# Kernel optimization log

Hardware: AMD Instinct MI355X
Metric: run time of the kernel (lower is better)

The kernel has to match this reference:

```python
import jax, jax.numpy as jnp
import numpy as np

WINDOW = 4
EPS = 1e-5


def setup_inputs() -> dict:
    key = jax.random.key(0)
    ks = jax.random.split(key, 12)
    B, T, D = 2, 4096, 1024
    H = D // 2
    s = 0.02
    return {
        "x": jax.random.normal(ks[0], (B, T, D), dtype=jnp.float32),
        # tension_net: Linear(2D -> D/2), SiLU, Linear(D/2 -> 1). Weights stored [in, out].
        "w1": jax.random.normal(ks[1], (2 * D, H), dtype=jnp.float32) * s,
        "b1": jnp.zeros((H,), dtype=jnp.float32),
        "w2": jax.random.normal(ks[2], (H, 1), dtype=jnp.float32) * s,
        "b2": jnp.zeros((1,), dtype=jnp.float32),
        # wv: Linear(D -> D)
        "wv_w": jax.random.normal(ks[3], (D, D), dtype=jnp.float32) * s,
        "wv_b": jnp.zeros((D,), dtype=jnp.float32),
        # merge: Linear(2D -> D)
        "merge_w": jax.random.normal(ks[4], (2 * D, D), dtype=jnp.float32) * s,
        "merge_b": jnp.zeros((D,), dtype=jnp.float32),
        # LayerNorm(D)
        "gamma": jnp.ones((D,), dtype=jnp.float32),
        "beta": jnp.zeros((D,), dtype=jnp.float32),
    }


def reference(x, w1, b1, w2, b2, wv_w, wv_b, merge_w, merge_b, gamma, beta):
    B, T, D = x.shape
    W = WINDOW
    # Causal sliding-window neighbor gather: nb[:, t, w] = x[:, t-w-1] if t-w-1 >= 0 else 0.
    idx = jnp.arange(T)[:, None] - jnp.arange(W)[None, :] - 1          # [T, W]
    valid = (idx >= 0)                                                  # [T, W]
    nb = jnp.take(x, jnp.clip(idx, 0, None), axis=1)                   # [B, T, W, D]
    nb = jnp.where(valid[None, :, :, None], nb, jnp.zeros((), x.dtype))
    # Pairwise tension gate: tiny MLP on [h_t, nb].
    h_t = jnp.broadcast_to(x[:, :, None, :], (B, T, W, D))
    pair = jnp.concatenate([h_t, nb], axis=-1)                          # [B, T, W, 2D]
    hid = jax.nn.silu(jnp.einsum('btwe,eh->btwh', pair, w1) + b1)       # [B, T, W, D/2]
    tau = jax.nn.sigmoid((jnp.einsum('btwh,ho->btwo', hid, w2) + b2)[..., 0])  # [B, T, W]
    # Value projection of neighbors (note: zero-padded neighbors still get wv bias, matching torch).
    v = jnp.einsum('btwd,de->btwe', nb, wv_w) + wv_b                    # [B, T, W, D]
    msg = jnp.einsum('btw,btwd->btd', tau, v)                           # [B, T, D]
    # Merge + LayerNorm.
    y = jnp.einsum('bte,ed->btd', jnp.concatenate([x, msg], axis=-1), merge_w) + merge_b
    mu = jnp.mean(y, axis=-1, keepdims=True)
    var = jnp.mean(jnp.square(y - mu), axis=-1, keepdims=True)
    y = (y - mu) * jax.lax.rsqrt(var + EPS) * gamma + beta
    return y
```

## Files before the change

### kernel.cpp

```cpp
#include <hip/hip_runtime.h>
#include <hip/hip_bf16.h>

#define TT 4096
#define TD 1024
#define TM 8192
#define CN 3072
#define EPS 1e-5f

typedef __bf16 bf16;
typedef __bf16 bf16x4 __attribute__((ext_vector_type(4)));
typedef __bf16 bf16x8 __attribute__((ext_vector_type(8)));
typedef float  f32x4  __attribute__((ext_vector_type(4)));

#define GLOBAL_AS __attribute__((address_space(1)))
#define LDS_AS    __attribute__((address_space(3)))

__global__ __launch_bounds__(256) void prep_kernel(const float* __restrict__ x,
                                                   const float* __restrict__ w1,
                                                   const float* __restrict__ wv_w,
                                                   const float* __restrict__ wv_b,
                                                   const float* __restrict__ merge_w,
                                                   bf16* __restrict__ Xbf,
                                                   bf16* __restrict__ BigBT,
                                                   bf16* __restrict__ Amb,
                                                   bf16* __restrict__ WvBf,
                                                   float* __restrict__ cvecP) {
    __shared__ float tile[32][33];
    int b = blockIdx.x;
    const int tid = threadIdx.x;

    if (b < 16) {
        const int j = (b & 3) * 256 + tid;
        const int e0 = (b >> 2) * 256;
        const float* col = merge_w + (size_t)(1024 + e0) * 1024 + j;
        float acc = 0.f;
#pragma unroll 32
        for (int e = 0; e < 256; ++e) acc += wv_b[e0 + e] * col[(size_t)e * 1024];
        cvecP[(b >> 2) * 1024 + j] = acc;
        return;
    }
    b -= 16;
    if (b < 8192) {
        int i = b * 256 + tid;
        float4 v = ((const float4*)x)[i];
        bf16x4 o; o[0] = (bf16)v.x; o[1] = (bf16)v.y; o[2] = (bf16)v.z; o[3] = (bf16)v.w;
        *(bf16x4*)(Xbf + (size_t)i * 4) = o;
        return;
    }
    b -= 8192;

    const float* src; bf16* dst; int srcN, tilesX, dstOff;
    if (b < 512)       {            src = w1;                        srcN = 512;  tilesX = 16; dst = BigBT; dstOff = 0;    }
    else if (b < 1024) { b -= 512;  src = w1 + (size_t)1024 * 512;   srcN = 512;  tilesX = 16; dst = BigBT; dstOff = 512;  }
    else if (b < 2048) { b -= 1024; src = merge_w;                   srcN = 1024; tilesX = 32; dst = BigBT; dstOff = 2048; }
    else if (b < 3072) { b -= 2048; src = merge_w + (size_t)1024 * 1024; srcN = 1024; tilesX = 32; dst = Amb; dstOff = 0; }
    else {
        b -= 3072;
        int i = b * 256 + tid;
        float4 v = ((const float4*)wv_w)[i];
        bf16x4 o; o[0] = (bf16)v.x; o[1] = (bf16)v.y; o[2] = (bf16)v.z; o[3] = (bf16)v.w;
        *(bf16x4*)(WvBf + (size_t)i * 4) = o;
        return;
    }
    int n0 = (b % tilesX) * 32, k0 = (b / tilesX) * 32;
    int tx = tid & 31, ty = tid >> 5;
#pragma unroll
    for (int r = 0; r < 32; r += 8)
        tile[ty + r][tx] = src[(size_t)(k0 + ty + r) * srcN + n0 + tx];
    __syncthreads();
#pragma unroll
    for (int r = 0; r < 32; r += 8)
        dst[(size_t)(dstOff + n0 + ty + r) * 1024 + k0 + tx] = (bf16)tile[tx][ty + r];
}

__global__ __launch_bounds__(256) void wprime_kernel(const bf16* __restrict__ Amb,
                                                     const bf16* __restrict__ WvBf,
                                                     bf16* __restrict__ Wout,
                                                     const float* __restrict__ cvecP,
                                                     float* __restrict__ cvec) {
    int b = blockIdx.x;
    if (b == 256) {
        int j = threadIdx.x * 4;
        float4 s0 = *(const float4*)(cvecP + j);
        float4 s1 = *(const float4*)(cvecP + 1024 + j);
        float4 s2 = *(const float4*)(cvecP + 2048 + j);
        float4 s3 = *(const float4*)(cvecP + 3072 + j);
        float4 o = {s0.x + s1.x + s2.x + s3.x, s0.y + s1.y + s2.y + s3.y,
                    s0.z + s1.z + s2.z + s3.z, s0.w + s1.w + s2.w + s3.w};
        *(float4*)(cvec + j) = o;
        return;
    }
    __shared__ bf16 As[64 * 64];
    __shared__ bf16 Bs[64 * 64];
    const int m0 = (b >> 4) * 64;
    const int n0 = (b & 15) * 64;
    const int tid = threadIdx.x;
    const int wave = tid >> 6, lane = tid & 63;
    const int wr = (wave >> 1) * 32, wc = (wave & 1) * 32;
    const int lrow = lane & 15, cbase = lane >> 4;
    const int sw = lrow & 7;

    f32x4 acc[2][2] = {};

    for (int k0 = 0; k0 < 1024; k0 += 64) {
        __syncthreads();
#pragma unroll
        for (int c = 0; c < 2; ++c) {
            int e = (c * 256 + tid) * 8;
            int row = e >> 6;
            int q = (e >> 3) & 7;
            int gcol = ((q ^ (row & 7)) << 3);
            const bf16* ga = Amb  + (size_t)(m0 + row) * 1024 + k0 + gcol;
            const bf16* gb = WvBf + (size_t)(n0 + row) * 1024 + k0 + gcol;
            __builtin_amdgcn_global_load_lds((const GLOBAL_AS void*)ga,
                                             (LDS_AS void*)(As + e), 16, 0, 0);
            __builtin_amdgcn_global_load_lds((const GLOBAL_AS void*)gb,
                                             (LDS_AS void*)(Bs + e), 16, 0, 0);
        }
        __syncthreads();

#pragma unroll
        for (int kk = 0; kk < 2; ++kk) {
            const int qo = ((cbase + kk * 4) ^ sw) << 3;
            bf16x8 af[2], bfr[2];
#pragma unroll
            for (int i = 0; i < 2; ++i) {
                af[i]  = *(const bf16x8*)(As + (wr + i * 16 + lrow) * 64 + qo);
                bfr[i] = *(const bf16x8*)(Bs + (wc + i * 16 + lrow) * 64 + qo);
            }
#pragma unroll
            for (int i = 0; i < 2; ++i)
#pragma unroll
                for (int j = 0; j < 2; ++j)
                    acc[i][j] = __builtin_amdgcn_mfma_f32_16x16x32_bf16(af[i], bfr[j], acc[i][j], 0, 0, 0);
        }
    }

    const int lr = (lane >> 4) * 4, lc = lane & 15;
#pragma unroll
    for (int i = 0; i < 2; ++i)
#pragma unroll
        for (int j = 0; j < 2; ++j)
#pragma unroll
            for (int r = 0; r < 4; ++r)
                Wout[(size_t)(m0 + wr + i * 16 + lr + r) * 1024 + (n0 + wc + j * 16 + lc)]
                    = (bf16)acc[i][j][r];
}

__global__ __launch_bounds__(256, 2) void gemm_big(const bf16* __restrict__ A,
                                                   const bf16* __restrict__ BT,
                                                   bf16* __restrict__ C) {
    __shared__ bf16 SMEM[28672];
    bf16* As = SMEM;
    bf16* Bs = SMEM + 16384;
    const int NB = 3072, K = 1024;

    int bx = blockIdx.x, by = blockIdx.y;
    {
        int L = by * 32 + bx;
        int xcd = L & 7, idx = L >> 3;
        by = xcd * 4 + (idx >> 5);
        bx = idx & 31;
    }
    const int m0 = by * 256;
    const int n0 = bx * 96;
    const int tid = threadIdx.x;
    const int wave = tid >> 6, lane = tid & 63;
    const int wr = wave * 64;
    const int lrow = lane & 15, cbase = lane >> 4;
    const int sw = lrow & 7;

    f32x4 acc[4][6] = {};

    for (int k0 = 0; k0 < K; k0 += 64) {
        __syncthreads();
#pragma unroll
        for (int c = 0; c < 11; ++c) {
            if (c < 8) {
                int e = (c * 256 + tid) * 8;
                int row = e >> 6;
                int q = (e >> 3) & 7;
                int gcol = ((q ^ (row & 7)) << 3);
                const bf16* ga = A + (size_t)(m0 + row) * K + k0 + gcol;
                __builtin_amdgcn_global_load_lds((const GLOBAL_AS void*)ga,
                                                 (LDS_AS void*)(As + e), 16, 0, 0);
            } else {
                int e = ((c - 8) * 256 + tid) * 8;
                int row = e >> 6;
                int q = (e >> 3) & 7;
                int gcol = ((q ^ (row & 7)) << 3);
                const bf16* gb = BT + (size_t)(n0 + row) * K + k0 + gcol;
                __builtin_amdgcn_global_load_lds((const GLOBAL_AS void*)gb,
                                                 (LDS_AS void*)(Bs + e), 16, 0, 0);
            }
        }
        __syncthreads();

#pragma unroll
        for (int kk = 0; kk < 2; ++kk) {
            const int qo = ((cbase + kk * 4) ^ sw) << 3;
            bf16x8 af[4], bfr[6];
#pragma unroll
            for (int i = 0; i < 4; ++i)
                af[i] = *(const bf16x8*)(As + (wr + i * 16 + lrow) * 64 + qo);
#pragma unroll
            for (int j = 0; j < 6; ++j)
                bfr[j] = *(const bf16x8*)(Bs + (j * 16 + lrow) * 64 + qo);
#pragma unroll
            for (int i = 0; i < 4; ++i)
#pragma unroll
                for (int j = 0; j < 6; ++j)
                    acc[i][j] = __builtin_amdgcn_mfma_f32_16x16x32_bf16(af[i], bfr[j], acc[i][j], 0, 0, 0);
        }
    }

    __syncthreads();
    bf16* ep = SMEM + wave * 6656;
    const int lr = (lane >> 4) * 4, lc = lane & 15;
#pragma unroll
    for (int i = 0; i < 4; ++i)
#pragma unroll
        for (int j = 0; j < 6; ++j)
#pragma unroll
            for (int r = 0; r < 4; ++r)
                ep[(i * 16 + lr + r) * 104 + (j * 16 + lc)] = (bf16)acc[i][j][r];
    __syncthreads();

    bf16* Cw = C + (size_t)(m0 + wr) * NB + n0;
#pragma unroll
    for (int p = 0; p < 8; ++p) {
        int R = p * 8 + (lane >> 3);
        int Ccol = (lane & 7) * 8;
        bf16x8 v = *(const bf16x8*)(ep + R * 104 + Ccol);
        *(bf16x8*)(Cw + (size_t)R * NB + Ccol) = v;
    }
#pragma unroll
    for (int p = 0; p < 4; ++p) {
        int R = p * 16 + (lane >> 2);
        int Ccol = 64 + (lane & 3) * 8;
        bf16x8 v = *(const bf16x8*)(ep + R * 104 + Ccol);
        *(bf16x8*)(Cw + (size_t)R * NB + Ccol) = v;
    }
}

__global__ __launch_bounds__(256) void final_kernel(const bf16* __restrict__ C,
                                                    const float* __restrict__ b1,
                                                    const float* __restrict__ b2,
                                                    const float* __restrict__ w2,
                                                    const float* __restrict__ cvec,
                                                    const float* __restrict__ merge_b,
                                                    const float* __restrict__ gamma,
                                                    const float* __restrict__ beta,
                                                    float* __restrict__ out) {
    const int wave = threadIdx.x >> 6, lane = threadIdx.x & 63;
    const int row = blockIdx.x * 4 + wave;
    const int t = row & (TT - 1);
    const bf16* Crow = C + (size_t)row * CN;

    const int h0 = lane * 8;
    bf16x8 u8 = *(const bf16x8*)(Crow + h0);
    float4 b1a = *(const float4*)(b1 + h0), b1b = *(const float4*)(b1 + h0 + 4);
    float4 w2a = *(const float4*)(w2 + h0), w2b = *(const float4*)(w2 + h0 + 4);
    float u[8] = {(float)u8[0] + b1a.x, (float)u8[1] + b1a.y,
                  (float)u8[2] + b1a.z, (float)u8[3] + b1a.w,
                  (float)u8[4] + b1b.x, (float)u8[5] + b1b.y,
                  (float)u8[6] + b1b.z, (float)u8[7] + b1b.w};
    const float w2v[8] = {w2a.x, w2a.y, w2a.z, w2a.w, w2b.x, w2b.y, w2b.z, w2b.w};

    float partial[4];
#pragma unroll
    for (int w = 0; w < 4; ++w) {
        float p = 0.f;
        if (t >= w + 1) {
            bf16x8 v8 = *(const bf16x8*)(C + (size_t)(row - w - 1) * CN + 512 + h0);
#pragma unroll
            for (int k = 0; k < 8; ++k) {
                float z = u[k] + (float)v8[k];
                p += (z / (1.f + __expf(-z))) * w2v[k];
            }
        } else {
#pragma unroll
            for (int k = 0; k < 8; ++k) {
                float z = u[k];
                p += (z / (1.f + __expf(-z))) * w2v[k];
            }
        }
        partial[w] = p;
    }
#pragma unroll
    for (int w = 0; w < 4; ++w)
#pragma unroll
        for (int off = 1; off < 64; off <<= 1)
            partial[w] += __shfl_xor(partial[w], off, 64);

    const float bias2 = b2[0];
    float taus[4];
#pragma unroll
    for (int w = 0; w < 4; ++w)
        taus[w] = 1.f / (1.f + __expf(-(partial[w] + bias2)));
    const float tsum = taus[0] + taus[1] + taus[2] + taus[3];

    const int d0 = lane * 16;
    bf16x8 y1a = *(const bf16x8*)(Crow + 2048 + d0);
    bf16x8 y1b = *(const bf16x8*)(Crow + 2048 + d0 + 8);
    float v[16];
#pragma unroll
    for (int k = 0; k < 8; ++k) { v[k] = (float)y1a[k]; v[8 + k] = (float)y1b[k]; }
#pragma unroll
    for (int q = 0; q < 4; ++q) {
        float4 cv = *(const float4*)(cvec + d0 + q * 4);
        float4 mb = *(const float4*)(merge_b + d0 + q * 4);
        v[q*4+0] += tsum * cv.x + mb.x; v[q*4+1] += tsum * cv.y + mb.y;
        v[q*4+2] += tsum * cv.z + mb.z; v[q*4+3] += tsum * cv.w + mb.w;
    }
#pragma unroll
    for (int w = 0; w < 4; ++w) {
        if (t >= w + 1) {
            const bf16* Pn = C + (size_t)(row - w - 1) * CN + 1024 + d0;
            bf16x8 pa = *(const bf16x8*)Pn;
            bf16x8 pb = *(const bf16x8*)(Pn + 8);
#pragma unroll
            for (int k = 0; k < 8; ++k) {
                v[k] += taus[w] * (float)pa[k];
                v[8 + k] += taus[w] * (float)pb[k];
            }
        }
    }

    float s = 0.f, ss = 0.f;
#pragma unroll
    for (int k = 0; k < 16; ++k) { s += v[k]; ss += v[k] * v[k]; }
#pragma unroll
    for (int off = 1; off < 64; off <<= 1) {
        s  += __shfl_xor(s, off, 64);
        ss += __shfl_xor(ss, off, 64);
    }
    const float mu = s * (1.f / TD);
    const float var = ss * (1.f / TD) - mu * mu;
    const float r = rsqrtf(var + EPS);

#pragma unroll
    for (int q = 0; q < 4; ++q) {
        float4 g  = *(const float4*)(gamma + d0 + q * 4);
        float4 bt = *(const float4*)(beta + d0 + q * 4);
        float4 o;
        o.x = (v[q*4+0] - mu) * r * g.x + bt.x;
        o.y = (v[q*4+1] - mu) * r * g.y + bt.y;
        o.z = (v[q*4+2] - mu) * r * g.z + bt.z;
        o.w = (v[q*4+3] - mu) * r * g.w + bt.w;
        *(float4*)(out + (size_t)row * TD + d0 + q * 4) = o;
    }
}

extern "C" void kernel_launch(void* const* d_in, const int* in_sizes, int n_in,
                              void* d_out, int out_size, void* d_ws, size_t ws_size,
                              hipStream_t stream) {
    const float* x       = (const float*)d_in[0];
    const float* w1      = (const float*)d_in[1];
    const float* b1      = (const float*)d_in[2];
    const float* w2      = (const float*)d_in[3];
    const float* b2      = (const float*)d_in[4];
    const float* wv_w    = (const float*)d_in[5];
    const float* wv_b    = (const float*)d_in[6];
    const float* merge_w = (const float*)d_in[7];
    const float* merge_b = (const float*)d_in[8];
    const float* gamma   = (const float*)d_in[9];
    const float* beta    = (const float*)d_in[10];
    float* out = (float*)d_out;

    char* ws = (char*)d_ws;
    bf16*  Xbf   = (bf16*)ws;  ws += (size_t)TM * 1024 * 2;
    bf16*  BigBT = (bf16*)ws;  ws += (size_t)CN * 1024 * 2;
    bf16*  Amb   = (bf16*)ws;  ws += (size_t)1024 * 1024 * 2;
    bf16*  WvBf  = (bf16*)ws;  ws += (size_t)1024 * 1024 * 2;
    float* cvecP = (float*)ws; ws += (size_t)4 * 1024 * 4;
    float* cvec  = (float*)ws; ws += (size_t)1024 * 4;
    bf16*  Cbuf  = (bf16*)ws;

    prep_kernel<<<12304, 256, 0, stream>>>(x, w1, wv_w, wv_b, merge_w,
                                           Xbf, BigBT, Amb, WvBf, cvecP);

    wprime_kernel<<<257, 256, 0, stream>>>(Amb, WvBf, BigBT + (size_t)1024 * 1024,
                                           cvecP, cvec);

    gemm_big<<<dim3(32, 32), 256, 0, stream>>>(Xbf, BigBT, Cbuf);

    final_kernel<<<TM / 4, 256, 0, stream>>>(Cbuf, b1, b2, w2, cvec, merge_b,
                                             gamma, beta, out);
}
```

Before: 197.2 us.

## Double-buffer big GEMM with 512-thread 256x192 tiles and phased prefetch

Rewrites the main bf16 GEMM to use 512-thread blocks computing 256x192 tiles with a 2x4 wave grid. A/B tiles are double-buffered in LDS and loaded with asynchronous global-to-LDS copies interleaved between MFMA phases, gated by explicit vmcnt waits and barriers, so loads overlap compute. It also uses setprio around MFMA bursts and a new XCD-aware tile mapping. In exchange, LDS use doubles, which may limit occupancy, and the hand-counted waitcnt schedule is fragile.

```diff
diff --git a/kernel.cpp b/kernel.cpp
--- a/kernel.cpp
+++ b/kernel.cpp
@@ -147,72 +147,117 @@
                     = (bf16)acc[i][j][r];
 }
 
-__global__ __launch_bounds__(256, 2) void gemm_big(const bf16* __restrict__ A,
+#define STAGE_A(T, kh) do {                                                       \
+    bf16* base_ = SMEM + ((T) & 1) * 16384 + (kh) * 8192;                         \
+    _Pragma("unroll")                                                             \
+    for (int ld = 0; ld < 2; ++ld) {                                              \
+        int e_ = (ld * 512 + tid) * 8;                                            \
+        int row_ = e_ >> 5;                                                       \
+        int q2_ = (e_ >> 3) & 3;                                                  \
+        int gcol_ = ((q2_ ^ (row_ & 3)) << 3);                                    \
+        const bf16* ga_ = A + (size_t)(m0 + row_) * K + (T) * 64 + (kh) * 32 + gcol_; \
+        __builtin_amdgcn_global_load_lds((const GLOBAL_AS void*)ga_,              \
+                                         (LDS_AS void*)(base_ + e_), 16, 0, 0);   \
+    } } while (0)
+
+#define STAGE_B(T) do {                                                           \
+    bf16* base_ = SMEM + 32768 + ((T) & 1) * 12288;                               \
+    _Pragma("unroll")                                                             \
+    for (int ld = 0; ld < 3; ++ld) {                                              \
+        int e_ = (ld * 512 + tid) * 8;                                            \
+        int row_ = e_ >> 6;                                                       \
+        int q_ = (e_ >> 3) & 7;                                                   \
+        int gcol_ = ((q_ ^ (row_ & 7)) << 3);                                     \
+        const bf16* gb_ = BT + (size_t)(n0 + row_) * K + (T) * 64 + gcol_;        \
+        __builtin_amdgcn_global_load_lds((const GLOBAL_AS void*)gb_,              \
+                                         (LDS_AS void*)(base_ + e_), 16, 0, 0);   \
+    } } while (0)
+
+#define NOSTAGE do {} while (0)
+#define NOGATE  do {} while (0)
+#define GATE2 do { asm volatile("s_waitcnt vmcnt(2)" ::: "memory");               \
+                   __builtin_amdgcn_sched_barrier(0); } while (0)
+#define GATE0 do { asm volatile("s_waitcnt vmcnt(0)" ::: "memory");               \
+                   __builtin_amdgcn_sched_barrier(0); } while (0)
+
+#define PHASE(tt, kk, ih, STAGE, GATE) do {                                       \
+    bf16x8 af0 = *(const bf16x8*)(SMEM + (tt) * 16384 + (kk) * 8192 +             \
+                                  (wm * 64 + (ih) * 32 + lrow) * 32 + aqo);       \
+    bf16x8 af1 = *(const bf16x8*)(SMEM + (tt) * 16384 + (kk) * 8192 +             \
+                                  (wm * 64 + (ih) * 32 + 16 + lrow) * 32 + aqo);  \
+    if ((ih) == 0) {                                                              \
+        _Pragma("unroll")                                                         \
+        for (int j = 0; j < 6; ++j)                                               \
+            bfr[j] = *(const bf16x8*)(SMEM + 32768 + (tt) * 12288 +               \
+                                      (wn * 96 + j * 16 + lrow) * 64 +            \
+                                      (((cbase + (kk) * 4) ^ sw) << 3));          \
+    }                                                                             \
+    STAGE;                                                                        \
+    __builtin_amdgcn_s_barrier();                                                 \
+    __builtin_amdgcn_sched_barrier(0);                                            \
+    __builtin_amdgcn_s_setprio(1);                                                \
+    _Pragma("unroll")                                                             \
+    for (int j = 0; j < 6; ++j) {                                                 \
+        acc[(ih) * 2][j]     = __builtin_amdgcn_mfma_f32_16x16x32_bf16(           \
+                                   af0, bfr[j], acc[(ih) * 2][j], 0, 0, 0);       \
+        acc[(ih) * 2 + 1][j] = __builtin_amdgcn_mfma_f32_16x16x32_bf16(           \
+                                   af1, bfr[j], acc[(ih) * 2 + 1][j], 0, 0, 0);   \
+    }                                                                             \
+    __builtin_amdgcn_s_setprio(0);                                                \
+    GATE;                                                                         \
+    __builtin_amdgcn_s_barrier();                                                 \
+    __builtin_amdgcn_sched_barrier(0);                                            \
+} while (0)
+
+__global__ __launch_bounds__(512, 2) void gemm_big(const bf16* __restrict__ A,
                                                    const bf16* __restrict__ BT,
                                                    bf16* __restrict__ C) {
-    __shared__ bf16 SMEM[28672];
-    bf16* As = SMEM;
-    bf16* Bs = SMEM + 16384;
+    __shared__ __align__(16) bf16 SMEM[57344];
     const int NB = 3072, K = 1024;
 
-    int bx = blockIdx.x, by = blockIdx.y;
-    {
-        int L = by * 32 + bx;
-        int xcd = L & 7, idx = L >> 3;
-        by = xcd * 4 + (idx >> 5);
-        bx = idx & 31;
-    }
-    const int m0 = by * 256;
-    const int n0 = bx * 96;
+    int L = blockIdx.y * 16 + blockIdx.x;
+    int tile = (L & 7) * 64 + (L >> 3);
+    const int m0 = (tile >> 4) * 256;
+    const int n0 = (tile & 15) * 192;
     const int tid = threadIdx.x;
     const int wave = tid >> 6, lane = tid & 63;
-    const int wr = wave * 64;
+    const int wm = wave >> 1;
+    const int wn = wave & 1;
     const int lrow = lane & 15, cbase = lane >> 4;
     const int sw = lrow & 7;
+    const int aqo = ((cbase ^ (lrow & 3)) << 3);
 
     f32x4 acc[4][6] = {};
-
-    for (int k0 = 0; k0 < K; k0 += 64) {
-        __syncthreads();
-#pragma unroll
-        for (int c = 0; c < 11; ++c) {
-            if (c < 8) {
-                int e = (c * 256 + tid) * 8;
-                int row = e >> 6;
-                int q = (e >> 3) & 7;
-                int gcol = ((q ^ (row & 7)) << 3);
-                const bf16* ga = A + (size_t)(m0 + row) * K + k0 + gcol;
-                __builtin_amdgcn_global_load_lds((const GLOBAL_AS void*)ga,
-                                                 (LDS_AS void*)(As + e), 16, 0, 0);
-            } else {
-                int e = ((c - 8) * 256 + tid) * 8;
-                int row = e >> 6;
-                int q = (e >> 3) & 7;
-                int gcol = ((q ^ (row & 7)) << 3);
-                const bf16* gb = BT + (size_t)(n0 + row) * K + k0 + gcol;
-                __builtin_amdgcn_global_load_lds((const GLOBAL_AS void*)gb,
-                                                 (LDS_AS void*)(Bs + e), 16, 0, 0);
-            }
-        }
-        __syncthreads();
-
-#pragma unroll
-        for (int kk = 0; kk < 2; ++kk) {
-            const int qo = ((cbase + kk * 4) ^ sw) << 3;
-            bf16x8 af[4], bfr[6];
-#pragma unroll
-            for (int i = 0; i < 4; ++i)
-                af[i] = *(const bf16x8*)(As + (wr + i * 16 + lrow) * 64 + qo);
-#pragma unroll
-            for (int j = 0; j < 6; ++j)
-                bfr[j] = *(const bf16x8*)(Bs + (j * 16 + lrow) * 64 + qo);
-#pragma unroll
-            for (int i = 0; i < 4; ++i)
-#pragma unroll
-                for (int j = 0; j < 6; ++j)
-                    acc[i][j] = __builtin_amdgcn_mfma_f32_16x16x32_bf16(af[i], bfr[j], acc[i][j], 0, 0, 0);
-        }
-    }
+    bf16x8 bfr[6];
+
+    STAGE_A(0, 0);
+    STAGE_A(0, 1);
+    STAGE_B(0);
+    STAGE_A(1, 0);
+    asm volatile("s_waitcnt vmcnt(2)" ::: "memory");
+    __builtin_amdgcn_sched_barrier(0);
+    __builtin_amdgcn_s_barrier();
+    __builtin_amdgcn_sched_barrier(0);
+
+    for (int i = 0; i < 7; ++i) {
+        const int t1 = 2 * i + 1, t2 = 2 * i + 2, t3 = 2 * i + 3;
+        PHASE(0, 0, 0, STAGE_A(t1, 1), NOGATE);
+        PHASE(0, 0, 1, STAGE_B(t1),    NOGATE);
+        PHASE(0, 1, 0, STAGE_A(t2, 0), NOGATE);
+        PHASE(0, 1, 1, NOSTAGE,        GATE2);
+        PHASE(1, 0, 0, STAGE_A(t2, 1), NOGATE);
+        PHASE(1, 0, 1, STAGE_B(t2),    NOGATE);
+        PHASE(1, 1, 0, STAGE_A(t3, 0), NOGATE);
+        PHASE(1, 1, 1, NOSTAGE,        GATE2);
+    }
+    PHASE(0, 0, 0, STAGE_A(15, 1), NOGATE);
+    PHASE(0, 0, 1, STAGE_B(15),    NOGATE);
+    PHASE(0, 1, 0, NOSTAGE,        NOGATE);
+    PHASE(0, 1, 1, NOSTAGE,        GATE0);
+    PHASE(1, 0, 0, NOSTAGE,        NOGATE);
+    PHASE(1, 0, 1, NOSTAGE,        NOGATE);
+    PHASE(1, 1, 0, NOSTAGE,        NOGATE);
+    PHASE(1, 1, 1, NOSTAGE,        NOGATE);
 
     __syncthreads();
     bf16* ep = SMEM + wave * 6656;
@@ -226,7 +271,7 @@
                 ep[(i * 16 + lr + r) * 104 + (j * 16 + lc)] = (bf16)acc[i][j][r];
     __syncthreads();
 
-    bf16* Cw = C + (size_t)(m0 + wr) * NB + n0;
+    bf16* Cw = C + (size_t)(m0 + wm * 64) * NB + n0 + wn * 96;
 #pragma unroll
     for (int p = 0; p < 8; ++p) {
         int R = p * 8 + (lane >> 3);
@@ -383,7 +428,7 @@
     wprime_kernel<<<257, 256, 0, stream>>>(Amb, WvBf, BigBT + (size_t)1024 * 1024,
                                            cvecP, cvec);
 
-    gemm_big<<<dim3(32, 32), 256, 0, stream>>>(Xbf, BigBT, Cbuf);
+    gemm_big<<<dim3(16, 32), 512, 0, stream>>>(Xbf, BigBT, Cbuf);
 
     final_kernel<<<TM / 4, 256, 0, stream>>>(Cbuf, b1, b2, w2, cvec, merge_b,
                                              gamma, beta, out);
```

New measurement: 202.7 us. 2.8% more time.
